# Performance work log

Hardware: AMD Instinct MI355X
Metric: run time of the kernel (lower is better)

## Reference

```python
import jax, jax.numpy as jnp
import numpy as np
import math

B, N, W = 8, 2048, 512

def setup_inputs() -> dict:
    key0 = jax.random.key(0)
    ks = jax.random.split(key0, 6)
    return {
        "query": jax.random.normal(ks[0], (B, N, W), dtype=jnp.float32),
        "key":   jax.random.normal(ks[1], (B, N, W), dtype=jnp.float32),
        "W1": jax.random.normal(ks[2], (W, W), dtype=jnp.float32) * (1.0 / math.sqrt(W)),
        "b1": jax.random.normal(ks[3], (W,), dtype=jnp.float32) * 0.01,
        "W2": jax.random.normal(ks[4], (W, W), dtype=jnp.float32) * (1.0 / math.sqrt(W)),
        "b2": jax.random.normal(ks[5], (W,), dtype=jnp.float32) * 0.01,
    }

def _attn(q, k, v):
    # scores: [B, N, N]
    d_k = q.shape[-1]
    scores = jnp.einsum('bnd,bmd->bnm', q, k) / jnp.sqrt(jnp.asarray(d_k, q.dtype))
    p = jax.nn.softmax(scores, axis=-1)
    return jnp.einsum('bnm,bmd->bnd', p, v)

def reference(query, key, W1, b1, W2, b2):
    # nn.Linear: x @ W.T + b
    q = jnp.einsum('bnd,ed->bne', query, W1) + b1
    k = jnp.einsum('bnd,ed->bne', key, W2) + b2
    x1 = _attn(q, k, q)  # attention(query, key, query)
    x2 = _attn(k, q, k)  # attention(key, query, key)
    return jnp.concatenate((x1, x2), axis=1)  # [B, 2N, W]
```

## Files before the change

kernel.cpp:

```cpp
#include <hip/hip_runtime.h>
#include <hip/hip_bf16.h>
#include <stdint.h>

typedef unsigned short ushort_t;
typedef __attribute__((ext_vector_type(8))) short short8;
typedef __attribute__((ext_vector_type(4))) short short4v;
typedef __attribute__((ext_vector_type(4))) float f32x4;

__device__ inline ushort_t f2bf(float x) {
  uint32_t u = __float_as_uint(x);
  u += 0x7fffu + ((u >> 16) & 1u);
  return (ushort_t)(u >> 16);
}
__device__ inline float bfu2f(uint32_t h) { return __uint_as_float(h << 16); }

__device__ inline uint32_t pk2bf(float a, float b) {
  __hip_bfloat162 h = __float22bfloat162_rn(make_float2(a, b));
  union { __hip_bfloat162 h2; uint32_t u; } cv; cv.h2 = h; return cv.u;
}

__device__ inline void gload_lds16(const void* g, void* l) {
  __builtin_amdgcn_global_load_lds((const __attribute__((address_space(1))) uint32_t*)g,
                                   (__attribute__((address_space(3))) uint32_t*)l, 16, 0, 0);
}

__global__ __launch_bounds__(256) void linear_kernel(
    const float* __restrict__ query, const float* __restrict__ key,
    const float* __restrict__ W1, const float* __restrict__ b1,
    const float* __restrict__ W2, const float* __restrict__ b2,
    ushort_t* __restrict__ q_bf, ushort_t* __restrict__ k_bf,
    ushort_t* __restrict__ qT, ushort_t* __restrict__ kT)
{
  __shared__ __attribute__((aligned(16))) char smraw[34816];
  float*    smF = (float*)smraw;
  ushort_t* smU = (ushort_t*)smraw;

  int bx = blockIdx.x;
  int which = bx >> 9, r2 = bx & 511, ct = r2 & 3, rt = r2 >> 2;
  const float* X    = which ? key : query;
  const float* Wm   = which ? W2  : W1;
  const float* bias = which ? b2  : b1;
  ushort_t* OUT  = which ? k_bf : q_bf;
  ushort_t* OUTT = which ? kT   : qT;

  int t = threadIdx.x, w = t >> 6, lane = t & 63, g = lane >> 4, m = lane & 15;
  int wr = (w >> 1) * 64, wc = (w & 1) * 64;
  int sr = lane >> 3, sp = lane & 7, sc = sp ^ sr;

  f32x4 zero = {0.f, 0.f, 0.f, 0.f};
  f32x4 acc[4][4];
#pragma unroll
  for (int i = 0; i < 4; ++i)
#pragma unroll
    for (int j = 0; j < 4; ++j) acc[i][j] = zero;

  for (int d0 = 0; d0 < 512; d0 += 32) {
    __syncthreads();
#pragma unroll
    for (int i = 0; i < 8; ++i) {
      int qi = w * 8 + i;
      const float* gsrc;
      float* ldst;
      if (qi < 16) {
        gsrc = X + (size_t)(rt * 128 + qi * 8 + sr) * 512 + d0 + sc * 4;
        ldst = smF + qi * 256;
      } else {
        int s = qi - 16;
        gsrc = Wm + (size_t)(ct * 128 + s * 8 + sr) * 512 + d0 + sc * 4;
        ldst = smF + 4096 + s * 256;
      }
      gload_lds16(gsrc, ldst);
    }
    __syncthreads();

    short8 a4[4], b4[4];
#pragma unroll
    for (int i = 0; i < 4; ++i) {
      int row = wr + 16 * i + m, r8 = row & 7;
      int base = (row >> 3) * 256 + r8 * 32;
      f32x4 lo = *(const f32x4*)&smF[base + (((2 * g)     ^ r8) * 4)];
      f32x4 hi = *(const f32x4*)&smF[base + (((2 * g + 1) ^ r8) * 4)];
      union { uint32_t u[4]; short8 s; } fr;
      fr.u[0] = pk2bf(lo[0], lo[1]); fr.u[1] = pk2bf(lo[2], lo[3]);
      fr.u[2] = pk2bf(hi[0], hi[1]); fr.u[3] = pk2bf(hi[2], hi[3]);
      a4[i] = fr.s;
    }
#pragma unroll
    for (int j = 0; j < 4; ++j) {
      int row = wc + 16 * j + m, r8 = row & 7;
      int base = 4096 + (row >> 3) * 256 + r8 * 32;
      f32x4 lo = *(const f32x4*)&smF[base + (((2 * g)     ^ r8) * 4)];
      f32x4 hi = *(const f32x4*)&smF[base + (((2 * g + 1) ^ r8) * 4)];
      union { uint32_t u[4]; short8 s; } fr;
      fr.u[0] = pk2bf(lo[0], lo[1]); fr.u[1] = pk2bf(lo[2], lo[3]);
      fr.u[2] = pk2bf(hi[0], hi[1]); fr.u[3] = pk2bf(hi[2], hi[3]);
      b4[j] = fr.s;
    }
#pragma unroll
    for (int i = 0; i < 4; ++i)
#pragma unroll
      for (int j = 0; j < 4; ++j)
        acc[i][j] = __builtin_amdgcn_mfma_f32_16x16x32_bf16(a4[i], b4[j], acc[i][j], 0, 0, 0);
  }
  __syncthreads();

  float bw[4];
#pragma unroll
  for (int j = 0; j < 4; ++j) bw[j] = bias[ct * 128 + wc + 16 * j + m];

#pragma unroll
  for (int j = 0; j < 4; ++j)
#pragma unroll
    for (int i = 0; i < 4; ++i) {
      f32x4 c4 = acc[i][j];
#pragma unroll
      for (int rr = 0; rr < 4; ++rr)
        smU[(wr + 16 * i + 4 * g + rr) * 136 + wc + 16 * j + m] = f2bf(c4[rr] + bw[j]);
    }
  __syncthreads();
  {
    int row = t >> 1, half = t & 1;
    size_t gb = (size_t)(rt * 128 + row) * 512 + ct * 128 + half * 64;
#pragma unroll
    for (int i = 0; i < 8; ++i)
      *(short8*)(OUT + gb + i * 8) = *(const short8*)&smU[row * 136 + half * 64 + i * 8];
  }
  __syncthreads();

#pragma unroll
  for (int j = 0; j < 4; ++j)
#pragma unroll
    for (int i = 0; i < 4; ++i) {
      f32x4 c4 = acc[i][j];
      short4v tv;
#pragma unroll
      for (int rr = 0; rr < 4; ++rr) tv[rr] = (short)f2bf(c4[rr] + bw[j]);
      *(short4v*)&smU[(wc + 16 * j + m) * 136 + wr + 16 * i + 4 * g] = tv;
    }
  __syncthreads();
  {
    int cC = t >> 1, half = t & 1;
    size_t b_ = (size_t)(rt >> 4);
    size_t gb = b_ * (512 * 2048) + (size_t)(ct * 128 + cC) * 2048
              + (size_t)(rt & 15) * 128 + half * 64;
#pragma unroll
    for (int i = 0; i < 8; ++i)
      *(short8*)(OUTT + gb + i * 8) = *(const short8*)&smU[cC * 136 + half * 64 + i * 8];
  }
}

__global__ __launch_bounds__(512) void attn_kernel(
    const ushort_t* __restrict__ qb, const ushort_t* __restrict__ kb_,
    const ushort_t* __restrict__ qT, const ushort_t* __restrict__ kT,
    float* __restrict__ out)
{
  extern __shared__ ushort_t sm[];
  const float CEXP = 1.4426950408889634f / 22.62741699796952f;

  int bx = blockIdx.x;
  int group = bx & 15, mtile = bx >> 4;
  int b = group >> 1, att = group & 1;
  const ushort_t* Qp = (att ? kb_ : qb) + (size_t)b * (2048 * 512);
  const ushort_t* Kp = (att ? qb  : kb_) + (size_t)b * (2048 * 512);
  const ushort_t* Vt = (att ? kT  : qT)  + (size_t)b * (512 * 2048);

  int t = threadIdx.x, w = t >> 6, lane = t & 63, g = lane >> 4, m = lane & 15;
  int qrow = mtile * 128 + w * 16 + m;
  int sw8  = ((g ^ ((m >> 1) & 3)) * 8);
  int srow = lane >> 2;
  int soff = ((lane & 3) ^ ((lane >> 3) & 3)) * 8;

  short8 qf[16];
#pragma unroll
  for (int ks = 0; ks < 16; ++ks)
    qf[ks] = *(const short8*)(Qp + (size_t)qrow * 512 + ks * 32 + g * 8);

  f32x4 zero = {0.f, 0.f, 0.f, 0.f};
  f32x4 acc[32];
#pragma unroll
  for (int dt = 0; dt < 32; ++dt) acc[dt] = zero;
  float l = 0.f;

  auto stage = [&](int buf, int kb) {
    ushort_t* base = sm + buf * 32768;
    const int kbase = kb * 32;
#pragma unroll
    for (int i = 0; i < 4; ++i) {
      int qi = w * 4 + i, ks = qi >> 1, tt2 = qi & 1;
      const ushort_t* gsrc = Kp + (size_t)(kbase + tt2 * 16 + srow) * 512 + ks * 32 + soff;
      gload_lds16(gsrc, base + ks * 1024 + tt2 * 512);
    }
#pragma unroll
    for (int i = 0; i < 4; ++i) {
      int qi = w * 4 + i;
      const ushort_t* gsrc = Vt + (size_t)(qi * 16 + srow) * 2048 + kbase + soff;
      gload_lds16(gsrc, base + 16384 + qi * 512);
    }
  };

  stage(0, 0);

  for (int kb = 0; kb < 64; ++kb) {
    int cur = kb & 1;
    __syncthreads();
    if (kb + 1 < 64) stage(1 - cur, kb + 1);
    const ushort_t* base = sm + cur * 32768;

    f32x4 T0 = zero, T1 = zero;
#pragma unroll
    for (int ks = 0; ks < 16; ++ks) {
      short8 k0 = *(const short8*)&base[ks * 1024 +       m * 32 + sw8];
      short8 k1 = *(const short8*)&base[ks * 1024 + 512 + m * 32 + sw8];
      T0 = __builtin_amdgcn_mfma_f32_16x16x32_bf16(k0, qf[ks], T0, 0, 0, 0);
      T1 = __builtin_amdgcn_mfma_f32_16x16x32_bf16(k1, qf[ks], T1, 0, 0, 0);
    }

    uint32_t h[8];
#pragma unroll
    for (int r = 0; r < 4; ++r) {
      float e0 = __builtin_amdgcn_exp2f(T0[r] * CEXP);
      float e1 = __builtin_amdgcn_exp2f(T1[r] * CEXP);
      h[r]     = f2bf(e0);
      h[4 + r] = f2bf(e1);
      l += bfu2f(h[r]) + bfu2f(h[4 + r]);
    }
    int dw0 = (int)(h[0] | (h[1] << 16));
    int dw1 = (int)(h[2] | (h[3] << 16));
    int dw2 = (int)(h[4] | (h[5] << 16));
    int dw3 = (int)(h[6] | (h[7] << 16));

    int sA = ((2 * g) & 3) * 16 + m, sB = sA + 16;
    int A0 = __shfl(dw0, sA, 64), A1 = __shfl(dw1, sA, 64);
    int A2 = __shfl(dw2, sA, 64), A3 = __shfl(dw3, sA, 64);
    int B0 = __shfl(dw0, sB, 64), B1 = __shfl(dw1, sB, 64);
    int B2 = __shfl(dw2, sB, 64), B3 = __shfl(dw3, sB, 64);
    bool hi = (g >= 2);
    union { int i4[4]; short8 s; } pu;
    pu.i4[0] = hi ? A2 : A0; pu.i4[1] = hi ? A3 : A1;
    pu.i4[2] = hi ? B2 : B0; pu.i4[3] = hi ? B3 : B1;
    short8 pfrag = pu.s;

#pragma unroll
    for (int dt = 0; dt < 32; ++dt) {
      short8 vf = *(const short8*)&base[16384 + dt * 512 + m * 32 + sw8];
      acc[dt] = __builtin_amdgcn_mfma_f32_16x16x32_bf16(vf, pfrag, acc[dt], 0, 0, 0);
    }
  }

  l += __shfl_xor(l, 16, 64);
  l += __shfl_xor(l, 32, 64);
  float inv = 1.0f / l;
  size_t orow = (size_t)b * 4096 + (size_t)att * 2048 + mtile * 128 + w * 16 + m;
  float* obase = out + orow * 512;
#pragma unroll
  for (int dt = 0; dt < 32; ++dt) {
    f32x4 v = acc[dt] * inv;
    *(f32x4*)(obase + dt * 16 + g * 4) = v;
  }
}

extern "C" void kernel_launch(void* const* d_in, const int* in_sizes, int n_in,
                              void* d_out, int out_size, void* d_ws, size_t ws_size,
                              hipStream_t stream) {
  const float* query = (const float*)d_in[0];
  const float* key   = (const float*)d_in[1];
  const float* W1    = (const float*)d_in[2];
  const float* b1    = (const float*)d_in[3];
  const float* W2    = (const float*)d_in[4];
  const float* b2    = (const float*)d_in[5];
  float* out = (float*)d_out;

  ushort_t* ws   = (ushort_t*)d_ws;
  ushort_t* q_bf = ws;
  ushort_t* k_bf = ws + 8388608;
  ushort_t* qT   = ws + 16777216;
  ushort_t* kT   = ws + 25165824;

  (void)hipFuncSetAttribute((const void*)attn_kernel,
                            hipFuncAttributeMaxDynamicSharedMemorySize, 131072);

  linear_kernel<<<1024, 256, 0, stream>>>(query, key, W1, b1, W2, b2,
                                          q_bf, k_bf, qT, kT);
  attn_kernel<<<256, 512, 131072, stream>>>(q_bf, k_bf, qT, kT, out);
}
```

Baseline: 331.9 us.

## Double-buffer linear GEMM loads and give each attention wave two query tiles

The linear projection kernel now double-buffers its K-slices in LDS, prefetching the next tile while the current one is converted and multiplied. The attention kernel halves its block to 4 waves, and each wave handles 32 query rows as two 16-row tiles. This lets every K and V fragment read from LDS feed two MFMAs, cutting LDS traffic per FLOP. The cost is doubled accumulator and Q-fragment registers per wave (about 256 accumulator VGPRs plus 128 for Q), which risks spills and lowers occupancy and latency hiding.

Measured after the change: 352.8 us. 1.06x slower.

```diff
diff --git a/kernel.cpp b/kernel.cpp
--- a/kernel.cpp
+++ b/kernel.cpp
@@ -24,14 +24,14 @@
                                    (__attribute__((address_space(3))) uint32_t*)l, 16, 0, 0);
 }
 
-__global__ __launch_bounds__(256) void linear_kernel(
+__global__ __launch_bounds__(256, 2) void linear_kernel(
     const float* __restrict__ query, const float* __restrict__ key,
     const float* __restrict__ W1, const float* __restrict__ b1,
     const float* __restrict__ W2, const float* __restrict__ b2,
     ushort_t* __restrict__ q_bf, ushort_t* __restrict__ k_bf,
     ushort_t* __restrict__ qT, ushort_t* __restrict__ kT)
 {
-  __shared__ __attribute__((aligned(16))) char smraw[34816];
+  __shared__ __attribute__((aligned(16))) char smraw[65536];
   float*    smF = (float*)smraw;
   ushort_t* smU = (ushort_t*)smraw;
 
@@ -54,8 +54,8 @@
 #pragma unroll
     for (int j = 0; j < 4; ++j) acc[i][j] = zero;
 
-  for (int d0 = 0; d0 < 512; d0 += 32) {
-    __syncthreads();
+  auto stage = [&](int bufsel, int d0) {
+    float* dstb = smF + bufsel * 8192;
 #pragma unroll
     for (int i = 0; i < 8; ++i) {
       int qi = w * 8 + i;
@@ -63,23 +63,30 @@
       float* ldst;
       if (qi < 16) {
         gsrc = X + (size_t)(rt * 128 + qi * 8 + sr) * 512 + d0 + sc * 4;
-        ldst = smF + qi * 256;
+        ldst = dstb + qi * 256;
       } else {
         int s = qi - 16;
         gsrc = Wm + (size_t)(ct * 128 + s * 8 + sr) * 512 + d0 + sc * 4;
-        ldst = smF + 4096 + s * 256;
+        ldst = dstb + 4096 + s * 256;
       }
       gload_lds16(gsrc, ldst);
     }
+  };
+
+  stage(0, 0);
+
+  for (int it = 0; it < 16; ++it) {
     __syncthreads();
+    if (it + 1 < 16) stage((it + 1) & 1, (it + 1) * 32);
+    const float* bF = smF + (it & 1) * 8192;
 
     short8 a4[4], b4[4];
 #pragma unroll
     for (int i = 0; i < 4; ++i) {
       int row = wr + 16 * i + m, r8 = row & 7;
       int base = (row >> 3) * 256 + r8 * 32;
-      f32x4 lo = *(const f32x4*)&smF[base + (((2 * g)     ^ r8) * 4)];
-      f32x4 hi = *(const f32x4*)&smF[base + (((2 * g + 1) ^ r8) * 4)];
+      f32x4 lo = *(const f32x4*)&bF[base + (((2 * g)     ^ r8) * 4)];
+      f32x4 hi = *(const f32x4*)&bF[base + (((2 * g + 1) ^ r8) * 4)];
       union { uint32_t u[4]; short8 s; } fr;
       fr.u[0] = pk2bf(lo[0], lo[1]); fr.u[1] = pk2bf(lo[2], lo[3]);
       fr.u[2] = pk2bf(hi[0], hi[1]); fr.u[3] = pk2bf(hi[2], hi[3]);
@@ -89,8 +96,8 @@
     for (int j = 0; j < 4; ++j) {
       int row = wc + 16 * j + m, r8 = row & 7;
       int base = 4096 + (row >> 3) * 256 + r8 * 32;
-      f32x4 lo = *(const f32x4*)&smF[base + (((2 * g)     ^ r8) * 4)];
-      f32x4 hi = *(const f32x4*)&smF[base + (((2 * g + 1) ^ r8) * 4)];
+      f32x4 lo = *(const f32x4*)&bF[base + (((2 * g)     ^ r8) * 4)];
+      f32x4 hi = *(const f32x4*)&bF[base + (((2 * g + 1) ^ r8) * 4)];
       union { uint32_t u[4]; short8 s; } fr;
       fr.u[0] = pk2bf(lo[0], lo[1]); fr.u[1] = pk2bf(lo[2], lo[3]);
       fr.u[2] = pk2bf(hi[0], hi[1]); fr.u[3] = pk2bf(hi[2], hi[3]);
@@ -149,7 +156,7 @@
   }
 }
 
-__global__ __launch_bounds__(512) void attn_kernel(
+__global__ __launch_bounds__(256, 1) void attn_kernel(
     const ushort_t* __restrict__ qb, const ushort_t* __restrict__ kb_,
     const ushort_t* __restrict__ qT, const ushort_t* __restrict__ kT,
     float* __restrict__ out)
@@ -165,61 +172,48 @@
   const ushort_t* Vt = (att ? kT  : qT)  + (size_t)b * (512 * 2048);
 
   int t = threadIdx.x, w = t >> 6, lane = t & 63, g = lane >> 4, m = lane & 15;
-  int qrow = mtile * 128 + w * 16 + m;
+  int qrow0 = mtile * 128 + w * 32 + m;
+  int qrow1 = qrow0 + 16;
   int sw8  = ((g ^ ((m >> 1) & 3)) * 8);
   int srow = lane >> 2;
   int soff = ((lane & 3) ^ ((lane >> 3) & 3)) * 8;
 
-  short8 qf[16];
-#pragma unroll
-  for (int ks = 0; ks < 16; ++ks)
-    qf[ks] = *(const short8*)(Qp + (size_t)qrow * 512 + ks * 32 + g * 8);
+  short8 qf0[16], qf1[16];
+#pragma unroll
+  for (int ks = 0; ks < 16; ++ks) {
+    qf0[ks] = *(const short8*)(Qp + (size_t)qrow0 * 512 + ks * 32 + g * 8);
+    qf1[ks] = *(const short8*)(Qp + (size_t)qrow1 * 512 + ks * 32 + g * 8);
+  }
 
   f32x4 zero = {0.f, 0.f, 0.f, 0.f};
-  f32x4 acc[32];
-#pragma unroll
-  for (int dt = 0; dt < 32; ++dt) acc[dt] = zero;
-  float l = 0.f;
+  f32x4 acc0[32], acc1[32];
+#pragma unroll
+  for (int dt = 0; dt < 32; ++dt) { acc0[dt] = zero; acc1[dt] = zero; }
+  float l0 = 0.f, l1 = 0.f;
 
   auto stage = [&](int buf, int kb) {
     ushort_t* base = sm + buf * 32768;
     const int kbase = kb * 32;
 #pragma unroll
-    for (int i = 0; i < 4; ++i) {
-      int qi = w * 4 + i, ks = qi >> 1, tt2 = qi & 1;
+    for (int i = 0; i < 8; ++i) {
+      int qi = w * 8 + i, ks = qi >> 1, tt2 = qi & 1;
       const ushort_t* gsrc = Kp + (size_t)(kbase + tt2 * 16 + srow) * 512 + ks * 32 + soff;
       gload_lds16(gsrc, base + ks * 1024 + tt2 * 512);
     }
 #pragma unroll
-    for (int i = 0; i < 4; ++i) {
-      int qi = w * 4 + i;
+    for (int i = 0; i < 8; ++i) {
+      int qi = w * 8 + i;
       const ushort_t* gsrc = Vt + (size_t)(qi * 16 + srow) * 2048 + kbase + soff;
       gload_lds16(gsrc, base + 16384 + qi * 512);
     }
   };
 
-  stage(0, 0);
-
-  for (int kb = 0; kb < 64; ++kb) {
-    int cur = kb & 1;
-    __syncthreads();
-    if (kb + 1 < 64) stage(1 - cur, kb + 1);
-    const ushort_t* base = sm + cur * 32768;
-
-    f32x4 T0 = zero, T1 = zero;
-#pragma unroll
-    for (int ks = 0; ks < 16; ++ks) {
-      short8 k0 = *(const short8*)&base[ks * 1024 +       m * 32 + sw8];
-      short8 k1 = *(const short8*)&base[ks * 1024 + 512 + m * 32 + sw8];
-      T0 = __builtin_amdgcn_mfma_f32_16x16x32_bf16(k0, qf[ks], T0, 0, 0, 0);
-      T1 = __builtin_amdgcn_mfma_f32_16x16x32_bf16(k1, qf[ks], T1, 0, 0, 0);
-    }
-
+  auto softpack = [&](const f32x4& Ta, const f32x4& Tb, float& l) -> short8 {
     uint32_t h[8];
 #pragma unroll
     for (int r = 0; r < 4; ++r) {
-      float e0 = __builtin_amdgcn_exp2f(T0[r] * CEXP);
-      float e1 = __builtin_amdgcn_exp2f(T1[r] * CEXP);
+      float e0 = __builtin_amdgcn_exp2f(Ta[r] * CEXP);
+      float e1 = __builtin_amdgcn_exp2f(Tb[r] * CEXP);
       h[r]     = f2bf(e0);
       h[4 + r] = f2bf(e1);
       l += bfu2f(h[r]) + bfu2f(h[4 + r]);
@@ -228,7 +222,6 @@
     int dw1 = (int)(h[2] | (h[3] << 16));
     int dw2 = (int)(h[4] | (h[5] << 16));
     int dw3 = (int)(h[6] | (h[7] << 16));
-
     int sA = ((2 * g) & 3) * 16 + m, sB = sA + 16;
     int A0 = __shfl(dw0, sA, 64), A1 = __shfl(dw1, sA, 64);
     int A2 = __shfl(dw2, sA, 64), A3 = __shfl(dw3, sA, 64);
@@ -238,24 +231,51 @@
     union { int i4[4]; short8 s; } pu;
     pu.i4[0] = hi ? A2 : A0; pu.i4[1] = hi ? A3 : A1;
     pu.i4[2] = hi ? B2 : B0; pu.i4[3] = hi ? B3 : B1;
-    short8 pfrag = pu.s;
+    return pu.s;
+  };
+
+  stage(0, 0);
+
+  for (int kb = 0; kb < 64; ++kb) {
+    int cur = kb & 1;
+    __syncthreads();
+    if (kb + 1 < 64) stage(1 - cur, kb + 1);
+    const ushort_t* base = sm + cur * 32768;
+
+    f32x4 T0 = zero, T1 = zero, T2 = zero, T3 = zero;
+#pragma unroll
+    for (int ks = 0; ks < 16; ++ks) {
+      short8 k0 = *(const short8*)&base[ks * 1024 +       m * 32 + sw8];
+      short8 k1 = *(const short8*)&base[ks * 1024 + 512 + m * 32 + sw8];
+      T0 = __builtin_amdgcn_mfma_f32_16x16x32_bf16(k0, qf0[ks], T0, 0, 0, 0);
+      T1 = __builtin_amdgcn_mfma_f32_16x16x32_bf16(k1, qf0[ks], T1, 0, 0, 0);
+      T2 = __builtin_amdgcn_mfma_f32_16x16x32_bf16(k0, qf1[ks], T2, 0, 0, 0);
+      T3 = __builtin_amdgcn_mfma_f32_16x16x32_bf16(k1, qf1[ks], T3, 0, 0, 0);
+    }
+
+    short8 pfrag0 = softpack(T0, T1, l0);
+    short8 pfrag1 = softpack(T2, T3, l1);
 
 #pragma unroll
     for (int dt = 0; dt < 32; ++dt) {
       short8 vf = *(const short8*)&base[16384 + dt * 512 + m * 32 + sw8];
-      acc[dt] = __builtin_amdgcn_mfma_f32_16x16x32_bf16(vf, pfrag, acc[dt], 0, 0, 0);
-    }
-  }
-
-  l += __shfl_xor(l, 16, 64);
-  l += __shfl_xor(l, 32, 64);
-  float inv = 1.0f / l;
-  size_t orow = (size_t)b * 4096 + (size_t)att * 2048 + mtile * 128 + w * 16 + m;
-  float* obase = out + orow * 512;
+      acc0[dt] = __builtin_amdgcn_mfma_f32_16x16x32_bf16(vf, pfrag0, acc0[dt], 0, 0, 0);
+      acc1[dt] = __builtin_amdgcn_mfma_f32_16x16x32_bf16(vf, pfrag1, acc1[dt], 0, 0, 0);
+    }
+  }
+
+  l0 += __shfl_xor(l0, 16, 64); l0 += __shfl_xor(l0, 32, 64);
+  l1 += __shfl_xor(l1, 16, 64); l1 += __shfl_xor(l1, 32, 64);
+  float inv0 = 1.0f / l0, inv1 = 1.0f / l1;
+  size_t orow0 = (size_t)b * 4096 + (size_t)att * 2048 + qrow0;
+  float* ob0 = out + orow0 * 512;
+  float* ob1 = ob0 + 16 * 512;
 #pragma unroll
   for (int dt = 0; dt < 32; ++dt) {
-    f32x4 v = acc[dt] * inv;
-    *(f32x4*)(obase + dt * 16 + g * 4) = v;
+    f32x4 v0 = acc0[dt] * inv0;
+    f32x4 v1 = acc1[dt] * inv1;
+    *(f32x4*)(ob0 + dt * 16 + g * 4) = v0;
+    *(f32x4*)(ob1 + dt * 16 + g * 4) = v1;
   }
 }
 
@@ -281,5 +301,5 @@
 
   linear_kernel<<<1024, 256, 0, stream>>>(query, key, W1, b1, W2, b2,
                                           q_bf, k_bf, qT, kT);
-  attn_kernel<<<256, 512, 131072, stream>>>(q_bf, k_bf, qT, kT, out);
-}
+  attn_kernel<<<256, 256, 131072, stream>>>(q_bf, k_bf, qT, kT, out);
+}
```
